# Kernel tuning notes

Hardware: AMD Instinct MI355X
Metric: run time of the kernel (lower is better)

## Reference

```python
import jax, jax.numpy as jnp
import numpy as np

BETA = 0.9
THRESHOLD = 1.0  # snntorch Leaky default threshold, reset_mechanism='subtract'
ALPHA = 2.0      # snntorch default ATan surrogate alpha (irrelevant for fwd)


def spike_fn(x):
    # Heaviside spike: fires when membrane exceeds threshold (x = mem - threshold)
    return (x > 0).astype(x.dtype)


def setup_inputs() -> dict:
    key = jax.random.key(0)
    k1, k2, k3 = jax.random.split(key, 3)
    T, B, NIN, HID = 1024, 128, 256, 1024
    # Bernoulli spike train input (the module consumes spikes)
    spike_seq = (jax.random.uniform(k1, (T, B, NIN)) < 0.2).astype(jnp.float32)
    # Xavier-uniform-ish init for fc1, scaled for fc2 (gain=0.5)
    lim1 = float(np.sqrt(6.0 / (NIN + HID)))
    W1 = jax.random.uniform(k2, (HID, NIN), minval=-lim1, maxval=lim1, dtype=jnp.float32)
    b1 = jnp.zeros((HID,), jnp.float32)
    lim2 = 0.5 * float(np.sqrt(6.0 / (HID + 2)))
    W2 = jax.random.uniform(k3, (2, HID), minval=-lim2, maxval=lim2, dtype=jnp.float32)
    # avoidance bias: +0.8 on first/second half columns (as in _init_weights)
    half = NIN // 2
    W2 = W2.at[1, :half].add(0.8)
    W2 = W2.at[0, half:NIN].add(0.8)
    b2 = jnp.zeros((2,), jnp.float32)
    return {"spike_seq": spike_seq, "W1": W1, "b1": b1, "W2": W2, "b2": b2}


def reference(spike_seq, W1, b1, W2, b2):
    T, B, _ = spike_seq.shape
    HID = W1.shape[0]
    mem1_0 = jnp.zeros((B, HID), spike_seq.dtype)
    mem2_0 = jnp.zeros((B, 2), spike_seq.dtype)

    def step(carry, x_t):
        mem1, mem2 = carry
        h = x_t @ W1.T + b1                      # [B, HID]
        mem1 = BETA * mem1 + h
        spk1 = spike_fn(mem1 - THRESHOLD)
        mem1 = mem1 - spk1 * THRESHOLD           # subtract reset
        h2 = spk1 @ W2.T + b2                    # [B, 2]
        mem2 = BETA * mem2 + h2
        spk2 = spike_fn(mem2 - THRESHOLD)
        mem2 = mem2 - spk2 * THRESHOLD
        return (mem1, mem2), (spk2, spk1)

    (mem1_f, mem2_f), (out_spikes, hidden_spikes) = jax.lax.scan(
        step, (mem1_0, mem2_0), spike_seq)
    return out_spikes, hidden_spikes, mem2_f
```

## Files before the change

kernel.cpp:

```cpp
#include <hip/hip_runtime.h>
#include <hip/hip_bf16.h>
#include <stdint.h>


#define TT  1024
#define BB  128
#define NIN 256
#define HID 1024

#define OFF_HID  262144ULL
#define OFF_MEM2 134479872ULL

__global__ __launch_bounds__(256) void k_transpose(const float* __restrict__ W1,
                                                   float* __restrict__ W1T) {
    int idx = blockIdx.x * 256 + threadIdx.x;
    int j = idx & (HID - 1);
    int i = idx >> 10;
    W1T[(size_t)i * HID + j] = W1[(size_t)j * NIN + i];
}

__global__ __launch_bounds__(256) void k_pack(const float* __restrict__ x,
                                              unsigned int* __restrict__ cntArr,
                                              unsigned char* __restrict__ idxArr,
                                              int slots) {
    size_t tb = blockIdx.x;
    int tid = threadIdx.x;
    int lane = tid & 63, w = tid >> 6;
    float v = x[tb * NIN + tid];
    bool act = v > 0.5f;
    unsigned long long m = __ballot(act);
    __shared__ unsigned int wc[4];
    __shared__ unsigned char sIdx[96];
    if (lane == 0) wc[w] = (unsigned int)__popcll(m);
    __syncthreads();
    unsigned int off = 0;
#pragma unroll
    for (int k = 0; k < 4; ++k) if (k < w) off += wc[k];
    unsigned int cnt = wc[0] + wc[1] + wc[2] + wc[3];
    unsigned int rank = off + (unsigned int)__popcll(m & ((1ull << lane) - 1));
    if (act && rank < (unsigned int)slots) sIdx[rank] = (unsigned char)tid;
    __syncthreads();
    if (tid * 4 < slots)
        ((unsigned int*)(idxArr + tb * (size_t)slots))[tid] = ((const unsigned int*)sIdx)[tid];
    if (tid == 0) cntArr[tb] = cnt;
}

__global__ __launch_bounds__(256) void k_snn(const float* __restrict__ W1T,
                                             const unsigned int* __restrict__ cntArr,
                                             const unsigned char* __restrict__ idxArr,
                                             const float* __restrict__ x,
                                             const float* __restrict__ b1,
                                             float* __restrict__ outHid,
                                             int slots) {
#pragma clang fp contract(off)
    const int jc   = blockIdx.x & 15;
    const int bg   = blockIdx.x >> 4;
    const int tid  = threadIdx.x;
    const int lane = tid & 63;
    const int wave = tid >> 6;
    const int b    = (bg << 2) + wave;
    const int q    = lane & 15;
    const int s    = lane >> 4;
    const int jq   = (jc << 6) + (q << 2);

    __shared__ float4 sW4[257 * 16];
    __shared__ float4 sEx[4][64];

    for (int p = tid; p < NIN * 16; p += 256) {
        int i = p >> 4, qq = p & 15;
        sW4[p] = *reinterpret_cast<const float4*>(W1T + (size_t)i * HID + (jc << 6) + (qq << 2));
    }
    if (tid < 16) sW4[256 * 16 + tid] = make_float4(0.f, 0.f, 0.f, 0.f);
    __syncthreads();

    float mem0 = 0.f, mem1 = 0.f, mem2 = 0.f, mem3 = 0.f;
    const float4 bs = *reinterpret_cast<const float4*>(b1 + jq);
    const int ub = __builtin_amdgcn_readfirstlane(b);
    const int sl = slots;
    const int dwTot = sl >> 2;
    int dwA = q;            if (dwA >= dwTot) dwA = dwTot - 1;
    int dwB = 16 + (q & 7); if (dwB >= dwTot) dwB = dwTot - 1;

    const bool sLo   = (s < 2);
    const bool sEven = ((s & 1) == 0);

    size_t tb0 = (size_t)s * BB + ub;
    unsigned int cnt_v = cntArr[tb0];
    {
        const unsigned int* lp = (const unsigned int*)(idxArr + tb0 * (size_t)sl);
    }
    unsigned int vA_v = ((const unsigned int*)(idxArr + tb0 * (size_t)sl))[dwA];
    unsigned int vB_v = ((const unsigned int*)(idxArr + tb0 * (size_t)sl))[dwB];

    for (int t = 0; t < TT; t += 4) {
        unsigned int cnt = cnt_v, vA = vA_v, vB = vB_v;

        int tn = (t + 4 < TT) ? t + 4 : t;
        size_t tbn = (size_t)(tn + s) * BB + ub;
        cnt_v = cntArr[tbn];
        const unsigned int* lpn = (const unsigned int*)(idxArr + tbn * (size_t)sl);
        vA_v = lpn[dwA];
        vB_v = lpn[dwB];

        unsigned int mylim = cnt < (unsigned int)sl ? cnt : (unsigned int)sl;
        int l0 = __builtin_amdgcn_readlane((int)mylim, 0);
        int l1 = __builtin_amdgcn_readlane((int)mylim, 16);
        int l2 = __builtin_amdgcn_readlane((int)mylim, 32);
        int l3 = __builtin_amdgcn_readlane((int)mylim, 48);
        int kmax = l0 > l1 ? l0 : l1;
        kmax = kmax > l2 ? kmax : l2;
        kmax = kmax > l3 ? kmax : l3;

        float4 e0, e1, e2, e3;

        if (!__any((int)(cnt > (unsigned int)sl))) {
            float h0 = bs.x, h1 = bs.y, h2 = bs.z, h3 = bs.w;
            int kA = kmax < 64 ? kmax : 64;
            for (int k = 0; k < kA; k += 4) {
                int w = k >> 2;
                unsigned d0 = (unsigned)__builtin_amdgcn_readlane((int)vA, w);
                unsigned d1 = (unsigned)__builtin_amdgcn_readlane((int)vA, 16 + w);
                unsigned d2 = (unsigned)__builtin_amdgcn_readlane((int)vA, 32 + w);
                unsigned d3 = (unsigned)__builtin_amdgcn_readlane((int)vA, 48 + w);
                unsigned dl = sEven ? d0 : d1;
                unsigned dh = sEven ? d2 : d3;
                unsigned d  = sLo ? dl : dh;
#pragma unroll
                for (int i2 = 0; i2 < 4; ++i2) {
                    unsigned row = ((unsigned)(k + i2) < mylim) ? ((d >> (8 * i2)) & 255u) : 256u;
                    float4 v = sW4[row * 16 + q];
                    h0 += v.x; h1 += v.y; h2 += v.z; h3 += v.w;
                }
            }
            for (int k = 64; k < kmax; k += 4) {
                int w = (k >> 2) - 16;
                unsigned d0 = (unsigned)__builtin_amdgcn_readlane((int)vB, w);
                unsigned d1 = (unsigned)__builtin_amdgcn_readlane((int)vB, 16 + w);
                unsigned d2 = (unsigned)__builtin_amdgcn_readlane((int)vB, 32 + w);
                unsigned d3 = (unsigned)__builtin_amdgcn_readlane((int)vB, 48 + w);
                unsigned dl = sEven ? d0 : d1;
                unsigned dh = sEven ? d2 : d3;
                unsigned d  = sLo ? dl : dh;
#pragma unroll
                for (int i2 = 0; i2 < 4; ++i2) {
                    unsigned row = ((unsigned)(k + i2) < mylim) ? ((d >> (8 * i2)) & 255u) : 256u;
                    float4 v = sW4[row * 16 + q];
                    h0 += v.x; h1 += v.y; h2 += v.z; h3 += v.w;
                }
            }
            sEx[wave][lane] = make_float4(h0, h1, h2, h3);
            e0 = sEx[wave][q];
            e1 = sEx[wave][16 + q];
            e2 = sEx[wave][32 + q];
            e3 = sEx[wave][48 + q];
        } else {
#pragma unroll
            for (int tt = 0; tt < 4; ++tt) {
                const float* xr = x + ((size_t)(t + tt) * BB + ub) * NIN;
                float g0 = bs.x, g1 = bs.y, g2 = bs.z, g3 = bs.w;
                for (int w2 = 0; w2 < 4; ++w2) {
                    unsigned long long m = __ballot(xr[(w2 << 6) + lane] > 0.5f);
                    while (m) {
                        int i = (w2 << 6) + __builtin_ctzll(m);
                        m &= m - 1;
                        float4 v = sW4[i * 16 + q];
                        g0 += v.x; g1 += v.y; g2 += v.z; g3 += v.w;
                    }
                }
                if      (tt == 0) e0 = make_float4(g0, g1, g2, g3);
                else if (tt == 1) e1 = make_float4(g0, g1, g2, g3);
                else if (tt == 2) e2 = make_float4(g0, g1, g2, g3);
                else              e3 = make_float4(g0, g1, g2, g3);
            }
        }

#define MSTEP(hv, memv, spv) { float mm_ = 0.9f * (memv); mm_ = mm_ + (hv);     \
        spv = (mm_ - 1.0f > 0.0f) ? 1.0f : 0.0f; memv = mm_ - spv; }
        float sA0, sA1, sA2, sA3, sB0, sB1, sB2, sB3;
        float sC0, sC1, sC2, sC3, sD0, sD1, sD2, sD3;
        MSTEP(e0.x, mem0, sA0) MSTEP(e0.y, mem1, sA1) MSTEP(e0.z, mem2, sA2) MSTEP(e0.w, mem3, sA3)
        MSTEP(e1.x, mem0, sB0) MSTEP(e1.y, mem1, sB1) MSTEP(e1.z, mem2, sB2) MSTEP(e1.w, mem3, sB3)
        MSTEP(e2.x, mem0, sC0) MSTEP(e2.y, mem1, sC1) MSTEP(e2.z, mem2, sC2) MSTEP(e2.w, mem3, sC3)
        MSTEP(e3.x, mem0, sD0) MSTEP(e3.y, mem1, sD1) MSTEP(e3.z, mem2, sD2) MSTEP(e3.w, mem3, sD3)
#undef MSTEP

        float4 sv;
        sv.x = sLo ? (sEven ? sA0 : sB0) : (sEven ? sC0 : sD0);
        sv.y = sLo ? (sEven ? sA1 : sB1) : (sEven ? sC1 : sD1);
        sv.z = sLo ? (sEven ? sA2 : sB2) : (sEven ? sC2 : sD2);
        sv.w = sLo ? (sEven ? sA3 : sB3) : (sEven ? sC3 : sD3);
        *reinterpret_cast<float4*>(outHid + ((size_t)(t + s) * BB + b) * HID + jq) = sv;
    }
}

__global__ __launch_bounds__(256) void k_h2(const float* __restrict__ spk,
                                            const float* __restrict__ W2,
                                            const float* __restrict__ b2,
                                            float* __restrict__ h2) {
#pragma clang fp contract(off)
    const int lane = threadIdx.x & 63;
    const int wave = threadIdx.x >> 6;
    size_t tb = (size_t)blockIdx.x * 4 + wave;
    const float* row = spk + tb * HID;
    float s0 = 0.0f, s1 = 0.0f;
#pragma unroll
    for (int c = 0; c < 16; ++c) {
        float v  = row[c * 64 + lane];
        float r0 = v * W2[c * 64 + lane];
        float r1 = v * W2[HID + c * 64 + lane];
#pragma unroll
        for (int off = 32; off > 0; off >>= 1) {
            r0 += __shfl_xor(r0, off, 64);
            r1 += __shfl_xor(r1, off, 64);
        }
        s0 += r0;
        s1 += r1;
    }
    s0 += b2[0];
    s1 += b2[1];
    if (lane == 0)
        *reinterpret_cast<float2*>(h2 + tb * 2) = make_float2(s0, s1);
}

__global__ __launch_bounds__(256) void k_scan(const float* __restrict__ h2,
                                              float* __restrict__ outSpk,
                                              float* __restrict__ outMem2) {
#pragma clang fp contract(off)
    const int tid = threadIdx.x;
    float mem = 0.0f;
    float cur[8], nxt[8];
#pragma unroll
    for (int k = 0; k < 8; ++k) cur[k] = h2[k * 256 + tid];
    for (int t0 = 0; t0 < TT; t0 += 8) {
#pragma unroll
        for (int k = 0; k < 8; ++k) {
            int tn = t0 + 8 + k;
            nxt[k] = (tn < TT) ? h2[tn * 256 + tid] : 0.0f;
        }
#pragma unroll
        for (int k = 0; k < 8; ++k) {
            float mm = 0.9f * mem;
            mm = mm + cur[k];
            float spk = (mm - 1.0f > 0.0f) ? 1.0f : 0.0f;
            mm = mm - spk;
            mem = mm;
            outSpk[(t0 + k) * 256 + tid] = spk;
        }
#pragma unroll
        for (int k = 0; k < 8; ++k) cur[k] = nxt[k];
    }
    outMem2[tid] = mem;
}

extern "C" void kernel_launch(void* const* d_in, const int* in_sizes, int n_in,
                              void* d_out, int out_size, void* d_ws, size_t ws_size,
                              hipStream_t stream) {
    const float* x  = (const float*)d_in[0];
    const float* W1 = (const float*)d_in[1];
    const float* b1 = (const float*)d_in[2];
    const float* W2 = (const float*)d_in[3];
    const float* b2 = (const float*)d_in[4];
    float* out = (float*)d_out;

    char* ws = (char*)d_ws;
    float*         W1T = (float*)(ws);
    unsigned int*  cnt = (unsigned int*)(ws + (1 << 20));
    unsigned char* idx = (unsigned char*)(ws + (1 << 20) + (1 << 19));

    size_t fixedB = (size_t)(1 << 20) + (1 << 19) + (1 << 20);
    size_t avail  = ws_size > fixedB ? ws_size - fixedB : 0;
    long   s      = (long)((avail / 131072) & ~(size_t)7);
    int slots = (int)(s > 96 ? 96 : (s < 8 ? 8 : s));

    float* h2 = (float*)(ws + (1 << 20) + (1 << 19) + (size_t)131072 * (size_t)slots);

    k_transpose<<<1024, 256, 0, stream>>>(W1, W1T);
    k_pack<<<131072, 256, 0, stream>>>(x, cnt, idx, slots);
    k_snn<<<512, 256, 0, stream>>>(W1T, cnt, idx, x, b1, out + OFF_HID, slots);
    k_h2<<<32768, 256, 0, stream>>>(out + OFF_HID, W2, b2, h2);
    k_scan<<<1, 256, 0, stream>>>(h2, out, out + OFF_MEM2);
}
```

Measured before the change: 1.233 ms.

## Split sparse W1 gather between LDS and global loads, peel predicated tails

The sparse accumulation loop now reads the first SPLIT dword-groups of spike indices from the LDS copy of W1T and the rest directly from global/L2 via a transposed W1T padded with a zero row 256. It also splits each range into unpredicated and predicated parts using the minimum count across the four lanes groups. Pointer arithmetic is reduced with incremental offsets, and occupancy is hinted with launch_bounds(256,2). The aim is to spread LDS bandwidth pressure onto the vector memory path and remove per-element predicate selects, at the cost of global-load latency inside the hot loop.

```diff
diff --git a/kernel.cpp b/kernel.cpp
--- a/kernel.cpp
+++ b/kernel.cpp
@@ -14,9 +14,10 @@
 __global__ __launch_bounds__(256) void k_transpose(const float* __restrict__ W1,
                                                    float* __restrict__ W1T) {
     int idx = blockIdx.x * 256 + threadIdx.x;
+    if (idx >= 257 * 1024) return;
     int j = idx & (HID - 1);
     int i = idx >> 10;
-    W1T[(size_t)i * HID + j] = W1[(size_t)j * NIN + i];
+    W1T[(size_t)i * HID + j] = (i < NIN) ? W1[(size_t)j * NIN + i] : 0.0f;
 }
 
 __global__ __launch_bounds__(256) void k_pack(const float* __restrict__ x,
@@ -45,13 +46,13 @@
     if (tid == 0) cntArr[tb] = cnt;
 }
 
-__global__ __launch_bounds__(256) void k_snn(const float* __restrict__ W1T,
-                                             const unsigned int* __restrict__ cntArr,
-                                             const unsigned char* __restrict__ idxArr,
-                                             const float* __restrict__ x,
-                                             const float* __restrict__ b1,
-                                             float* __restrict__ outHid,
-                                             int slots) {
+__global__ __launch_bounds__(256, 2) void k_snn(const float* __restrict__ W1T,
+                                                const unsigned int* __restrict__ cntArr,
+                                                const unsigned char* __restrict__ idxArr,
+                                                const float* __restrict__ x,
+                                                const float* __restrict__ b1,
+                                                float* __restrict__ outHid,
+                                                int slots) {
 #pragma clang fp contract(off)
     const int jc   = blockIdx.x & 15;
     const int bg   = blockIdx.x >> 4;
@@ -83,71 +84,104 @@
 
     const bool sLo   = (s < 2);
     const bool sEven = ((s & 1) == 0);
-
-    size_t tb0 = (size_t)s * BB + ub;
-    unsigned int cnt_v = cntArr[tb0];
-    {
-        const unsigned int* lp = (const unsigned int*)(idxArr + tb0 * (size_t)sl);
-    }
-    unsigned int vA_v = ((const unsigned int*)(idxArr + tb0 * (size_t)sl))[dwA];
-    unsigned int vB_v = ((const unsigned int*)(idxArr + tb0 * (size_t)sl))[dwB];
+    const float* wrow = W1T + jq;
+
+    unsigned offCnt = (unsigned)((s * BB + ub) * 4);
+    unsigned offA   = (unsigned)((s * BB + ub) * sl + dwA * 4);
+    unsigned offB   = (unsigned)((s * BB + ub) * sl + dwB * 4);
+    const unsigned stC = (unsigned)(4 * BB * 4);
+    const unsigned stL = (unsigned)(4 * BB * sl);
+
+    unsigned cnt_v = *(const unsigned*)((const char*)cntArr + offCnt);
+    unsigned vA_v  = *(const unsigned*)(idxArr + offA);
+    unsigned vB_v  = *(const unsigned*)(idxArr + offB);
+
+    float* outP = outHid + ((size_t)s * BB + b) * HID + jq;
+    const size_t outStep = (size_t)4 * BB * HID;
+
+#define RL(v, l) ((unsigned)__builtin_amdgcn_readlane((int)(v), (l)))
+#define FETCH_D(kd, dOut) do {                                                  \
+        unsigned _d0, _d1, _d2, _d3;                                            \
+        if ((kd) < 16) {                                                        \
+            _d0 = RL(vA, (kd));      _d1 = RL(vA, 16 + (kd));                   \
+            _d2 = RL(vA, 32 + (kd)); _d3 = RL(vA, 48 + (kd));                   \
+        } else { int _m = (kd) - 16;                                            \
+            _d0 = RL(vB, _m);        _d1 = RL(vB, 16 + _m);                     \
+            _d2 = RL(vB, 32 + _m);   _d3 = RL(vB, 48 + _m); }                   \
+        unsigned _dl = sEven ? _d0 : _d1;                                       \
+        unsigned _dh = sEven ? _d2 : _d3;                                       \
+        dOut = sLo ? _dl : _dh;                                                 \
+    } while (0)
+
+#define B_LDS(kd, PRED) do {                                                    \
+        unsigned d_; FETCH_D(kd, d_);                                           \
+        int kb_ = (kd) << 2;                                                    \
+        _Pragma("unroll")                                                       \
+        for (int i2 = 0; i2 < 4; ++i2) {                                        \
+            unsigned row_ = (d_ >> (8 * i2)) & 255u;                            \
+            if (PRED) row_ = ((unsigned)(kb_ + i2) < mylim) ? row_ : 256u;      \
+            float4 v_ = sW4[row_ * 16 + q];                                     \
+            h0 += v_.x; h1 += v_.y; h2 += v_.z; h3 += v_.w;                     \
+        }                                                                       \
+    } while (0)
+
+#define B_GLB(kd, PRED) do {                                                    \
+        unsigned d_; FETCH_D(kd, d_);                                           \
+        int kb_ = (kd) << 2;                                                    \
+        float4 va_, vb_, vc_, vd_;                                              \
+        unsigned r0_ = d_ & 255u, r1_ = (d_ >> 8) & 255u;                       \
+        unsigned r2_ = (d_ >> 16) & 255u, r3_ = d_ >> 24;                       \
+        if (PRED) {                                                             \
+            r0_ = ((unsigned)(kb_    ) < mylim) ? r0_ : 256u;                   \
+            r1_ = ((unsigned)(kb_ + 1) < mylim) ? r1_ : 256u;                   \
+            r2_ = ((unsigned)(kb_ + 2) < mylim) ? r2_ : 256u;                   \
+            r3_ = ((unsigned)(kb_ + 3) < mylim) ? r3_ : 256u;                   \
+        }                                                                       \
+        va_ = *reinterpret_cast<const float4*>(wrow + (size_t)r0_ * HID);       \
+        vb_ = *reinterpret_cast<const float4*>(wrow + (size_t)r1_ * HID);       \
+        vc_ = *reinterpret_cast<const float4*>(wrow + (size_t)r2_ * HID);       \
+        vd_ = *reinterpret_cast<const float4*>(wrow + (size_t)r3_ * HID);       \
+        h0 += va_.x; h1 += va_.y; h2 += va_.z; h3 += va_.w;                     \
+        h0 += vb_.x; h1 += vb_.y; h2 += vb_.z; h3 += vb_.w;                     \
+        h0 += vc_.x; h1 += vc_.y; h2 += vc_.z; h3 += vc_.w;                     \
+        h0 += vd_.x; h1 += vd_.y; h2 += vd_.z; h3 += vd_.w;                     \
+    } while (0)
+
+    const int SPLIT = 10;
 
     for (int t = 0; t < TT; t += 4) {
-        unsigned int cnt = cnt_v, vA = vA_v, vB = vB_v;
-
-        int tn = (t + 4 < TT) ? t + 4 : t;
-        size_t tbn = (size_t)(tn + s) * BB + ub;
-        cnt_v = cntArr[tbn];
-        const unsigned int* lpn = (const unsigned int*)(idxArr + tbn * (size_t)sl);
-        vA_v = lpn[dwA];
-        vB_v = lpn[dwB];
-
-        unsigned int mylim = cnt < (unsigned int)sl ? cnt : (unsigned int)sl;
+        unsigned cnt = cnt_v, vA = vA_v, vB = vB_v;
+
+        unsigned st = (t + 4 < TT) ? 1u : 0u;
+        offCnt += st * stC; offA += st * stL; offB += st * stL;
+        cnt_v = *(const unsigned*)((const char*)cntArr + offCnt);
+        vA_v  = *(const unsigned*)(idxArr + offA);
+        vB_v  = *(const unsigned*)(idxArr + offB);
+
+        unsigned mylim = cnt < (unsigned)sl ? cnt : (unsigned)sl;
         int l0 = __builtin_amdgcn_readlane((int)mylim, 0);
         int l1 = __builtin_amdgcn_readlane((int)mylim, 16);
         int l2 = __builtin_amdgcn_readlane((int)mylim, 32);
         int l3 = __builtin_amdgcn_readlane((int)mylim, 48);
-        int kmax = l0 > l1 ? l0 : l1;
-        kmax = kmax > l2 ? kmax : l2;
-        kmax = kmax > l3 ? kmax : l3;
+        int kmax = l0 > l1 ? l0 : l1; kmax = kmax > l2 ? kmax : l2; kmax = kmax > l3 ? kmax : l3;
+        int kmin = l0 < l1 ? l0 : l1; kmin = kmin < l2 ? kmin : l2; kmin = kmin < l3 ? kmin : l3;
+
+        int dwEnd = (kmax + 3) >> 2;
+        int dwMin = kmin >> 2;
+        int dwL   = dwEnd < SPLIT ? dwEnd : SPLIT;
+        int dwLm  = dwMin < dwL ? dwMin : dwL;
+        int dwGm  = dwMin < dwEnd ? dwMin : dwEnd;
+        if (dwGm < SPLIT) dwGm = SPLIT;
 
         float4 e0, e1, e2, e3;
 
-        if (!__any((int)(cnt > (unsigned int)sl))) {
+        if (!__any((int)(cnt > (unsigned)sl))) {
             float h0 = bs.x, h1 = bs.y, h2 = bs.z, h3 = bs.w;
-            int kA = kmax < 64 ? kmax : 64;
-            for (int k = 0; k < kA; k += 4) {
-                int w = k >> 2;
-                unsigned d0 = (unsigned)__builtin_amdgcn_readlane((int)vA, w);
-                unsigned d1 = (unsigned)__builtin_amdgcn_readlane((int)vA, 16 + w);
-                unsigned d2 = (unsigned)__builtin_amdgcn_readlane((int)vA, 32 + w);
-                unsigned d3 = (unsigned)__builtin_amdgcn_readlane((int)vA, 48 + w);
-                unsigned dl = sEven ? d0 : d1;
-                unsigned dh = sEven ? d2 : d3;
-                unsigned d  = sLo ? dl : dh;
-#pragma unroll
-                for (int i2 = 0; i2 < 4; ++i2) {
-                    unsigned row = ((unsigned)(k + i2) < mylim) ? ((d >> (8 * i2)) & 255u) : 256u;
-                    float4 v = sW4[row * 16 + q];
-                    h0 += v.x; h1 += v.y; h2 += v.z; h3 += v.w;
-                }
-            }
-            for (int k = 64; k < kmax; k += 4) {
-                int w = (k >> 2) - 16;
-                unsigned d0 = (unsigned)__builtin_amdgcn_readlane((int)vB, w);
-                unsigned d1 = (unsigned)__builtin_amdgcn_readlane((int)vB, 16 + w);
-                unsigned d2 = (unsigned)__builtin_amdgcn_readlane((int)vB, 32 + w);
-                unsigned d3 = (unsigned)__builtin_amdgcn_readlane((int)vB, 48 + w);
-                unsigned dl = sEven ? d0 : d1;
-                unsigned dh = sEven ? d2 : d3;
-                unsigned d  = sLo ? dl : dh;
-#pragma unroll
-                for (int i2 = 0; i2 < 4; ++i2) {
-                    unsigned row = ((unsigned)(k + i2) < mylim) ? ((d >> (8 * i2)) & 255u) : 256u;
-                    float4 v = sW4[row * 16 + q];
-                    h0 += v.x; h1 += v.y; h2 += v.z; h3 += v.w;
-                }
-            }
+            for (int kd = 0;     kd < dwLm;  ++kd) B_LDS(kd, false);
+            for (int kd = dwLm;  kd < dwL;   ++kd) B_LDS(kd, true);
+            for (int kd = SPLIT; kd < dwGm;  ++kd) B_GLB(kd, false);
+            for (int kd = dwGm;  kd < dwEnd; ++kd) B_GLB(kd, true);
+
             sEx[wave][lane] = make_float4(h0, h1, h2, h3);
             e0 = sEx[wave][q];
             e1 = sEx[wave][16 + q];
@@ -189,8 +223,13 @@
         sv.y = sLo ? (sEven ? sA1 : sB1) : (sEven ? sC1 : sD1);
         sv.z = sLo ? (sEven ? sA2 : sB2) : (sEven ? sC2 : sD2);
         sv.w = sLo ? (sEven ? sA3 : sB3) : (sEven ? sC3 : sD3);
-        *reinterpret_cast<float4*>(outHid + ((size_t)(t + s) * BB + b) * HID + jq) = sv;
+        *reinterpret_cast<float4*>(outP) = sv;
+        outP += outStep;
     }
+#undef B_GLB
+#undef B_LDS
+#undef FETCH_D
+#undef RL
 }
 
 __global__ __launch_bounds__(256) void k_h2(const float* __restrict__ spk,
@@ -264,17 +303,17 @@
 
     char* ws = (char*)d_ws;
     float*         W1T = (float*)(ws);
-    unsigned int*  cnt = (unsigned int*)(ws + (1 << 20));
-    unsigned char* idx = (unsigned char*)(ws + (1 << 20) + (1 << 19));
-
-    size_t fixedB = (size_t)(1 << 20) + (1 << 19) + (1 << 20);
+    unsigned int*  cnt = (unsigned int*)(ws + (2 << 20));
+    unsigned char* idx = (unsigned char*)(ws + (2 << 20) + (1 << 19));
+
+    size_t fixedB = (size_t)(2 << 20) + (1 << 19) + (1 << 20);
     size_t avail  = ws_size > fixedB ? ws_size - fixedB : 0;
     long   s      = (long)((avail / 131072) & ~(size_t)7);
     int slots = (int)(s > 96 ? 96 : (s < 8 ? 8 : s));
 
-    float* h2 = (float*)(ws + (1 << 20) + (1 << 19) + (size_t)131072 * (size_t)slots);
-
-    k_transpose<<<1024, 256, 0, stream>>>(W1, W1T);
+    float* h2 = (float*)(ws + (2 << 20) + (1 << 19) + (size_t)131072 * (size_t)slots);
+
+    k_transpose<<<1028, 256, 0, stream>>>(W1, W1T);
     k_pack<<<131072, 256, 0, stream>>>(x, cnt, idx, slots);
     k_snn<<<512, 256, 0, stream>>>(W1T, cnt, idx, x, b1, out + OFF_HID, slots);
     k_h2<<<32768, 256, 0, stream>>>(out + OFF_HID, W2, b2, h2);
```

Result: no change. 1.249 ms (+1.3%).
